# Performance work log

Hardware: AMD Instinct MI355X
Metric: run time of the kernel (lower is better)

## Reference

```python
import jax, jax.numpy as jnp
import numpy as np


def _piecewise_weights(gt):
    # stats over gt[0,0]; torch.std uses ddof=1
    g00 = gt[0, 0]
    gmin = jnp.min(g00)
    gmean = jnp.mean(g00)
    gmax = jnp.max(g00)
    sd = jnp.std(g00, ddof=1)
    m1 = gmean + sd
    m2 = gmean + 3.0 * sd
    w_low = (gt - gmin) / (m1 - gmin) * 0.2
    w_mid = (gt - m1) / (m2 - m1) * 0.5 + 0.2
    w_high = (gt - m2) / (gmax - m2) * 0.3 + 0.7
    return jnp.where(gt <= m1, w_low, jnp.where(gt <= m2, w_mid, w_high))


def setup_inputs() -> dict:
    key = jax.random.key(0)
    k1, k2 = jax.random.split(key)
    shape = (1, 1, 4096, 4096)
    inputs = jax.random.normal(k1, shape, dtype=jnp.float32)
    targets = jax.random.normal(k2, shape, dtype=jnp.float32)
    return {"inputs": inputs, "targets": targets}


def reference(inputs, targets):
    # gt is a detached clone of targets -> no grad through the weights
    gt = jax.lax.stop_gradient(targets)
    weights = _piecewise_weights(gt)
    loss = jnp.abs(targets - inputs)
    return jnp.mean(loss * weights)
```

## Files before the change

kernel.cpp:

```cpp
#include <hip/hip_runtime.h>
#include <math.h>

#define BS 256
#define NB 2048
#define NWAVES (BS / 64)
#define TBS 1024
#define TNW (TBS / 64)

__device__ inline double wred_sum(double v) {
#pragma unroll
    for (int o = 32; o > 0; o >>= 1) v += __shfl_down(v, o, 64);
    return v;
}
__device__ inline float wred_min(float v) {
#pragma unroll
    for (int o = 32; o > 0; o >>= 1) v = fminf(v, __shfl_down(v, o, 64));
    return v;
}
__device__ inline float wred_max(float v) {
#pragma unroll
    for (int o = 32; o > 0; o >>= 1) v = fmaxf(v, __shfl_down(v, o, 64));
    return v;
}

__global__ void __launch_bounds__(BS) k_stats(
        const float* __restrict__ t, int n,
        double* __restrict__ bsum, double* __restrict__ bss,
        float* __restrict__ bmn, float* __restrict__ bmx) {
    int tid = blockIdx.x * BS + threadIdx.x;
    const int stride = NB * BS;
    int n4 = n >> 2;
    const float4* t4 = (const float4*)t;

    double s = 0.0, ss = 0.0;
    float mn = 3.4e38f, mx = -3.4e38f;
    int i = tid;
    for (; i + stride < n4; i += 2 * stride) {
        float4 a = t4[i];
        float4 b = t4[i + stride];
        mn = fminf(mn, fminf(fminf(a.x, a.y), fminf(a.z, a.w)));
        mx = fmaxf(mx, fmaxf(fmaxf(a.x, a.y), fmaxf(a.z, a.w)));
        s += (double)a.x + (double)a.y + (double)a.z + (double)a.w;
        ss += (double)a.x * a.x + (double)a.y * a.y
            + (double)a.z * a.z + (double)a.w * a.w;
        mn = fminf(mn, fminf(fminf(b.x, b.y), fminf(b.z, b.w)));
        mx = fmaxf(mx, fmaxf(fmaxf(b.x, b.y), fmaxf(b.z, b.w)));
        s += (double)b.x + (double)b.y + (double)b.z + (double)b.w;
        ss += (double)b.x * b.x + (double)b.y * b.y
            + (double)b.z * b.z + (double)b.w * b.w;
    }
    for (; i < n4; i += stride) {
        float4 a = t4[i];
        mn = fminf(mn, fminf(fminf(a.x, a.y), fminf(a.z, a.w)));
        mx = fmaxf(mx, fmaxf(fmaxf(a.x, a.y), fmaxf(a.z, a.w)));
        s += (double)a.x + (double)a.y + (double)a.z + (double)a.w;
        ss += (double)a.x * a.x + (double)a.y * a.y
            + (double)a.z * a.z + (double)a.w * a.w;
    }
    if (tid == 0) {
        for (int j = (n4 << 2); j < n; j++) {
            float v = t[j];
            mn = fminf(mn, v); mx = fmaxf(mx, v);
            s += v; ss += (double)v * v;
        }
    }

    s = wred_sum(s); ss = wred_sum(ss); mn = wred_min(mn); mx = wred_max(mx);

    __shared__ double sh_s[NWAVES], sh_ss[NWAVES];
    __shared__ float sh_mn[NWAVES], sh_mx[NWAVES];
    int wid = threadIdx.x >> 6, lane = threadIdx.x & 63;
    if (lane == 0) { sh_s[wid] = s; sh_ss[wid] = ss; sh_mn[wid] = mn; sh_mx[wid] = mx; }
    __syncthreads();
    if (threadIdx.x == 0) {
        double S = sh_s[0], SS = sh_ss[0];
        float MN = sh_mn[0], MX = sh_mx[0];
        for (int k = 1; k < NWAVES; k++) {
            S += sh_s[k]; SS += sh_ss[k];
            MN = fminf(MN, sh_mn[k]); MX = fmaxf(MX, sh_mx[k]);
        }
        bsum[blockIdx.x] = S; bss[blockIdx.x] = SS;
        bmn[blockIdx.x] = MN; bmx[blockIdx.x] = MX;
    }
}

__device__ inline float welem(float g, float x, float gmin, float m1, float m2,
                              float sl, float sm, float shv) {
    float w = (g <= m1) ? (g - gmin) * sl
            : (g <= m2) ? (g - m1) * sm + 0.2f
                        : (g - m2) * shv + 0.7f;
    return fabsf(g - x) * w;
}

__global__ void __launch_bounds__(BS) k_loss(
        const float* __restrict__ x, const float* __restrict__ t, int n,
        const double* __restrict__ sbsum, const double* __restrict__ sbss,
        const float* __restrict__ sbmn, const float* __restrict__ sbmx,
        double* __restrict__ bsum) {
    __shared__ double sh_s[NWAVES], sh_ss[NWAVES];
    __shared__ float sh_mn[NWAVES], sh_mx[NWAVES];
    __shared__ float s_c[8];
    {
        double s = 0.0, ss = 0.0;
        float mn = 3.4e38f, mx = -3.4e38f;
        for (int i = threadIdx.x; i < NB; i += BS) {
            s += sbsum[i]; ss += sbss[i];
            mn = fminf(mn, sbmn[i]); mx = fmaxf(mx, sbmx[i]);
        }
        s = wred_sum(s); ss = wred_sum(ss); mn = wred_min(mn); mx = wred_max(mx);
        int wid = threadIdx.x >> 6, lane = threadIdx.x & 63;
        if (lane == 0) { sh_s[wid] = s; sh_ss[wid] = ss; sh_mn[wid] = mn; sh_mx[wid] = mx; }
        __syncthreads();
        if (threadIdx.x == 0) {
            double S = sh_s[0], SS = sh_ss[0];
            float MN = sh_mn[0], MX = sh_mx[0];
            for (int k = 1; k < NWAVES; k++) {
                S += sh_s[k]; SS += sh_ss[k];
                MN = fminf(MN, sh_mn[k]); MX = fmaxf(MX, sh_mx[k]);
            }
            double dn = (double)n;
            double mean = S / dn;
            double var = (SS - S * S / dn) / (dn - 1.0);
            double sd = sqrt(var);
            float m1 = (float)(mean + sd);
            float m2 = (float)(mean + 3.0 * sd);
            s_c[0] = MN;
            s_c[1] = m1;
            s_c[2] = m2;
            s_c[3] = 0.2f / (m1 - MN);
            s_c[4] = 0.5f / (m2 - m1);
            s_c[5] = 0.3f / (MX - m2);
        }
        __syncthreads();
    }
    float gmin = s_c[0], m1 = s_c[1], m2 = s_c[2];
    float sl = s_c[3], sm = s_c[4], shv = s_c[5];

    int tid = blockIdx.x * BS + threadIdx.x;
    const int stride = NB * BS;
    int n4 = n >> 2;
    const float4* x4 = (const float4*)x;
    const float4* t4 = (const float4*)t;

    double acc = 0.0;
    int i = tid;
    for (; i + stride < n4; i += 2 * stride) {
        float4 tv = t4[i], xv = x4[i];
        float4 tw = t4[i + stride], xw = x4[i + stride];
        float e0 = welem(tv.x, xv.x, gmin, m1, m2, sl, sm, shv);
        float e1 = welem(tv.y, xv.y, gmin, m1, m2, sl, sm, shv);
        float e2 = welem(tv.z, xv.z, gmin, m1, m2, sl, sm, shv);
        float e3 = welem(tv.w, xv.w, gmin, m1, m2, sl, sm, shv);
        acc += (double)e0 + (double)e1 + (double)e2 + (double)e3;
        float f0 = welem(tw.x, xw.x, gmin, m1, m2, sl, sm, shv);
        float f1 = welem(tw.y, xw.y, gmin, m1, m2, sl, sm, shv);
        float f2 = welem(tw.z, xw.z, gmin, m1, m2, sl, sm, shv);
        float f3 = welem(tw.w, xw.w, gmin, m1, m2, sl, sm, shv);
        acc += (double)f0 + (double)f1 + (double)f2 + (double)f3;
    }
    for (; i < n4; i += stride) {
        float4 tv = t4[i], xv = x4[i];
        float e0 = welem(tv.x, xv.x, gmin, m1, m2, sl, sm, shv);
        float e1 = welem(tv.y, xv.y, gmin, m1, m2, sl, sm, shv);
        float e2 = welem(tv.z, xv.z, gmin, m1, m2, sl, sm, shv);
        float e3 = welem(tv.w, xv.w, gmin, m1, m2, sl, sm, shv);
        acc += (double)e0 + (double)e1 + (double)e2 + (double)e3;
    }
    if (tid == 0) {
        for (int j = (n4 << 2); j < n; j++)
            acc += (double)welem(t[j], x[j], gmin, m1, m2, sl, sm, shv);
    }

    acc = wred_sum(acc);
    __shared__ double sh_acc[NWAVES];
    int wid = threadIdx.x >> 6, lane = threadIdx.x & 63;
    if (lane == 0) sh_acc[wid] = acc;
    __syncthreads();
    if (threadIdx.x == 0) {
        double S = sh_acc[0];
        for (int k = 1; k < NWAVES; k++) S += sh_acc[k];
        bsum[blockIdx.x] = S;
    }
}

__global__ void __launch_bounds__(TBS) k_final(
        const double* __restrict__ bsum, long long n, float* __restrict__ out) {
    double s = 0.0;
    for (int i = threadIdx.x; i < NB; i += TBS) s += bsum[i];
    s = wred_sum(s);
    __shared__ double sh_s[TNW];
    int wid = threadIdx.x >> 6, lane = threadIdx.x & 63;
    if (lane == 0) sh_s[wid] = s;
    __syncthreads();
    if (threadIdx.x == 0) {
        double S = sh_s[0];
        for (int i = 1; i < TNW; i++) S += sh_s[i];
        out[0] = (float)(S / (double)n);
    }
}

extern "C" void kernel_launch(void* const* d_in, const int* in_sizes, int n_in,
                              void* d_out, int out_size, void* d_ws, size_t ws_size,
                              hipStream_t stream) {
    const float* inp = (const float*)d_in[0];
    const float* tgt = (const float*)d_in[1];
    int n = in_sizes[0];

    char* ws = (char*)d_ws;
    double* sum1  = (double*)(ws);
    double* ss1   = (double*)(ws + 16384);
    float*  mn1   = (float*)(ws + 32768);
    float*  mx1   = (float*)(ws + 40960);
    double* sum2  = (double*)(ws + 49280);

    k_stats<<<NB, BS, 0, stream>>>(tgt, n, sum1, ss1, mn1, mx1);
    k_loss<<<NB, BS, 0, stream>>>(inp, tgt, n, sum1, ss1, mn1, mx1, sum2);
    k_final<<<1, TBS, 0, stream>>>(sum2, (long long)n, (float*)d_out);
}
```

Before: 46.64 us.

## Fuse final reduction into loss kernel via fixed-point slotted atomics

Removes the third k_final launch. Each loss block adds its partial sum as a fixed-point integer into one of 64 padded atomic slots and bumps a per-slot counter. The last block to arrive in each slot waits until all counters sum to the block count, then reduces the slots and writes the output. The grid is also halved to 1024 blocks with a 4x unrolled load loop, and the slots are zeroed by block 0 of the stats kernel. This trades a kernel launch for atomic traffic and a spin-wait, and the fixed-point scaling limits precision and range.

After: 46.95 us. No clear change (+0.7%).

```diff
diff --git a/kernel.cpp b/kernel.cpp
--- a/kernel.cpp
+++ b/kernel.cpp
@@ -2,10 +2,12 @@
 #include <math.h>
 
 #define BS 256
-#define NB 2048
+#define NBLK 1024
 #define NWAVES (BS / 64)
-#define TBS 1024
-#define TNW (TBS / 64)
+#define NSLOT 64
+#define PER_SLOT (NBLK / NSLOT)
+#define FXS 4294967296.0
+
 
 __device__ inline double wred_sum(double v) {
 #pragma unroll
@@ -21,41 +23,49 @@
 #pragma unroll
     for (int o = 32; o > 0; o >>= 1) v = fmaxf(v, __shfl_down(v, o, 64));
     return v;
+}
+
+__device__ inline void acc_stats(float4 v, double& s, double& ss, float& mn, float& mx) {
+    mn = fminf(mn, fminf(fminf(v.x, v.y), fminf(v.z, v.w)));
+    mx = fmaxf(mx, fmaxf(fmaxf(v.x, v.y), fmaxf(v.z, v.w)));
+    s += (double)v.x + (double)v.y + (double)v.z + (double)v.w;
+    ss += (double)v.x * v.x + (double)v.y * v.y
+        + (double)v.z * v.z + (double)v.w * v.w;
 }
 
 __global__ void __launch_bounds__(BS) k_stats(
         const float* __restrict__ t, int n,
         double* __restrict__ bsum, double* __restrict__ bss,
-        float* __restrict__ bmn, float* __restrict__ bmx) {
+        float* __restrict__ bmn, float* __restrict__ bmx,
+        char* __restrict__ slots) {
+    if (blockIdx.x == 0) {
+        if (threadIdx.x < NSLOT)
+            *(long long*)(slots + (size_t)threadIdx.x * 128) = 0ll;
+        else if (threadIdx.x < 2 * NSLOT)
+            *(unsigned*)(slots + 8192 + (size_t)(threadIdx.x - NSLOT) * 128) = 0u;
+    }
+
     int tid = blockIdx.x * BS + threadIdx.x;
-    const int stride = NB * BS;
+    const int stride = NBLK * BS;
     int n4 = n >> 2;
     const float4* t4 = (const float4*)t;
 
     double s = 0.0, ss = 0.0;
     float mn = 3.4e38f, mx = -3.4e38f;
     int i = tid;
-    for (; i + stride < n4; i += 2 * stride) {
+    for (; i + 3 * stride < n4; i += 4 * stride) {
         float4 a = t4[i];
         float4 b = t4[i + stride];
-        mn = fminf(mn, fminf(fminf(a.x, a.y), fminf(a.z, a.w)));
-        mx = fmaxf(mx, fmaxf(fmaxf(a.x, a.y), fmaxf(a.z, a.w)));
-        s += (double)a.x + (double)a.y + (double)a.z + (double)a.w;
-        ss += (double)a.x * a.x + (double)a.y * a.y
-            + (double)a.z * a.z + (double)a.w * a.w;
-        mn = fminf(mn, fminf(fminf(b.x, b.y), fminf(b.z, b.w)));
-        mx = fmaxf(mx, fmaxf(fmaxf(b.x, b.y), fmaxf(b.z, b.w)));
-        s += (double)b.x + (double)b.y + (double)b.z + (double)b.w;
-        ss += (double)b.x * b.x + (double)b.y * b.y
-            + (double)b.z * b.z + (double)b.w * b.w;
+        float4 c = t4[i + 2 * stride];
+        float4 d = t4[i + 3 * stride];
+        acc_stats(a, s, ss, mn, mx);
+        acc_stats(b, s, ss, mn, mx);
+        acc_stats(c, s, ss, mn, mx);
+        acc_stats(d, s, ss, mn, mx);
     }
     for (; i < n4; i += stride) {
         float4 a = t4[i];
-        mn = fminf(mn, fminf(fminf(a.x, a.y), fminf(a.z, a.w)));
-        mx = fmaxf(mx, fmaxf(fmaxf(a.x, a.y), fmaxf(a.z, a.w)));
-        s += (double)a.x + (double)a.y + (double)a.z + (double)a.w;
-        ss += (double)a.x * a.x + (double)a.y * a.y
-            + (double)a.z * a.z + (double)a.w * a.w;
+        acc_stats(a, s, ss, mn, mx);
     }
     if (tid == 0) {
         for (int j = (n4 << 2); j < n; j++) {
@@ -96,14 +106,15 @@
         const float* __restrict__ x, const float* __restrict__ t, int n,
         const double* __restrict__ sbsum, const double* __restrict__ sbss,
         const float* __restrict__ sbmn, const float* __restrict__ sbmx,
-        double* __restrict__ bsum) {
+        char* __restrict__ slots, float* __restrict__ out) {
     __shared__ double sh_s[NWAVES], sh_ss[NWAVES];
     __shared__ float sh_mn[NWAVES], sh_mx[NWAVES];
     __shared__ float s_c[8];
     {
         double s = 0.0, ss = 0.0;
         float mn = 3.4e38f, mx = -3.4e38f;
-        for (int i = threadIdx.x; i < NB; i += BS) {
+#pragma unroll 4
+        for (int i = threadIdx.x; i < NBLK; i += BS) {
             s += sbsum[i]; ss += sbss[i];
             mn = fminf(mn, sbmn[i]); mx = fmaxf(mx, sbmx[i]);
         }
@@ -137,34 +148,47 @@
     float sl = s_c[3], sm = s_c[4], shv = s_c[5];
 
     int tid = blockIdx.x * BS + threadIdx.x;
-    const int stride = NB * BS;
+    const int stride = NBLK * BS;
     int n4 = n >> 2;
     const float4* x4 = (const float4*)x;
     const float4* t4 = (const float4*)t;
 
     double acc = 0.0;
     int i = tid;
-    for (; i + stride < n4; i += 2 * stride) {
-        float4 tv = t4[i], xv = x4[i];
-        float4 tw = t4[i + stride], xw = x4[i + stride];
-        float e0 = welem(tv.x, xv.x, gmin, m1, m2, sl, sm, shv);
-        float e1 = welem(tv.y, xv.y, gmin, m1, m2, sl, sm, shv);
-        float e2 = welem(tv.z, xv.z, gmin, m1, m2, sl, sm, shv);
-        float e3 = welem(tv.w, xv.w, gmin, m1, m2, sl, sm, shv);
+    for (; i + 3 * stride < n4; i += 4 * stride) {
+        float4 t0 = t4[i];
+        float4 t1 = t4[i + stride];
+        float4 t2 = t4[i + 2 * stride];
+        float4 t3 = t4[i + 3 * stride];
+        float4 x0 = x4[i];
+        float4 x1 = x4[i + stride];
+        float4 x2 = x4[i + 2 * stride];
+        float4 x3 = x4[i + 3 * stride];
+        float e0 = welem(t0.x, x0.x, gmin, m1, m2, sl, sm, shv)
+                 + welem(t0.y, x0.y, gmin, m1, m2, sl, sm, shv)
+                 + welem(t0.z, x0.z, gmin, m1, m2, sl, sm, shv)
+                 + welem(t0.w, x0.w, gmin, m1, m2, sl, sm, shv);
+        float e1 = welem(t1.x, x1.x, gmin, m1, m2, sl, sm, shv)
+                 + welem(t1.y, x1.y, gmin, m1, m2, sl, sm, shv)
+                 + welem(t1.z, x1.z, gmin, m1, m2, sl, sm, shv)
+                 + welem(t1.w, x1.w, gmin, m1, m2, sl, sm, shv);
+        float e2 = welem(t2.x, x2.x, gmin, m1, m2, sl, sm, shv)
+                 + welem(t2.y, x2.y, gmin, m1, m2, sl, sm, shv)
+                 + welem(t2.z, x2.z, gmin, m1, m2, sl, sm, shv)
+                 + welem(t2.w, x2.w, gmin, m1, m2, sl, sm, shv);
+        float e3 = welem(t3.x, x3.x, gmin, m1, m2, sl, sm, shv)
+                 + welem(t3.y, x3.y, gmin, m1, m2, sl, sm, shv)
+                 + welem(t3.z, x3.z, gmin, m1, m2, sl, sm, shv)
+                 + welem(t3.w, x3.w, gmin, m1, m2, sl, sm, shv);
         acc += (double)e0 + (double)e1 + (double)e2 + (double)e3;
-        float f0 = welem(tw.x, xw.x, gmin, m1, m2, sl, sm, shv);
-        float f1 = welem(tw.y, xw.y, gmin, m1, m2, sl, sm, shv);
-        float f2 = welem(tw.z, xw.z, gmin, m1, m2, sl, sm, shv);
-        float f3 = welem(tw.w, xw.w, gmin, m1, m2, sl, sm, shv);
-        acc += (double)f0 + (double)f1 + (double)f2 + (double)f3;
     }
     for (; i < n4; i += stride) {
         float4 tv = t4[i], xv = x4[i];
-        float e0 = welem(tv.x, xv.x, gmin, m1, m2, sl, sm, shv);
-        float e1 = welem(tv.y, xv.y, gmin, m1, m2, sl, sm, shv);
-        float e2 = welem(tv.z, xv.z, gmin, m1, m2, sl, sm, shv);
-        float e3 = welem(tv.w, xv.w, gmin, m1, m2, sl, sm, shv);
-        acc += (double)e0 + (double)e1 + (double)e2 + (double)e3;
+        float e0 = welem(tv.x, xv.x, gmin, m1, m2, sl, sm, shv)
+                 + welem(tv.y, xv.y, gmin, m1, m2, sl, sm, shv)
+                 + welem(tv.z, xv.z, gmin, m1, m2, sl, sm, shv)
+                 + welem(tv.w, xv.w, gmin, m1, m2, sl, sm, shv);
+        acc += (double)e0;
     }
     if (tid == 0) {
         for (int j = (n4 << 2); j < n; j++)
@@ -173,29 +197,44 @@
 
     acc = wred_sum(acc);
     __shared__ double sh_acc[NWAVES];
+    __shared__ int s_fin;
     int wid = threadIdx.x >> 6, lane = threadIdx.x & 63;
     if (lane == 0) sh_acc[wid] = acc;
     __syncthreads();
     if (threadIdx.x == 0) {
         double S = sh_acc[0];
         for (int k = 1; k < NWAVES; k++) S += sh_acc[k];
-        bsum[blockIdx.x] = S;
-    }
-}
-
-__global__ void __launch_bounds__(TBS) k_final(
-        const double* __restrict__ bsum, long long n, float* __restrict__ out) {
-    double s = 0.0;
-    for (int i = threadIdx.x; i < NB; i += TBS) s += bsum[i];
-    s = wred_sum(s);
-    __shared__ double sh_s[TNW];
-    int wid = threadIdx.x >> 6, lane = threadIdx.x & 63;
-    if (lane == 0) sh_s[wid] = s;
+        int slot = blockIdx.x & (NSLOT - 1);
+        long long* lslot = (long long*)(slots + (size_t)slot * 128);
+        unsigned*  cslot = (unsigned*)(slots + 8192 + (size_t)slot * 128);
+        __hip_atomic_fetch_add(lslot, (long long)llrint(S * FXS),
+                               __ATOMIC_RELAXED, __HIP_MEMORY_SCOPE_AGENT);
+        asm volatile("s_waitcnt vmcnt(0)" ::: "memory");
+        unsigned prev = __hip_atomic_fetch_add(cslot, 1u,
+                               __ATOMIC_RELAXED, __HIP_MEMORY_SCOPE_AGENT);
+        s_fin = (prev == PER_SLOT - 1) ? 1 : 0;
+    }
     __syncthreads();
-    if (threadIdx.x == 0) {
-        double S = sh_s[0];
-        for (int i = 1; i < TNW; i++) S += sh_s[i];
-        out[0] = (float)(S / (double)n);
+    if (!s_fin) return;
+
+    if (threadIdx.x < 64) {
+        unsigned total;
+        do {
+            unsigned c = __hip_atomic_load(
+                (unsigned*)(slots + 8192 + (size_t)threadIdx.x * 128),
+                __ATOMIC_RELAXED, __HIP_MEMORY_SCOPE_AGENT);
+#pragma unroll
+            for (int o = 32; o > 0; o >>= 1) c += __shfl_down(c, o, 64);
+            total = __shfl(c, 0, 64);
+            if (total != NBLK) __builtin_amdgcn_s_sleep(32);
+        } while (total != NBLK);
+        long long v = __hip_atomic_load(
+            (long long*)(slots + (size_t)threadIdx.x * 128),
+            __ATOMIC_RELAXED, __HIP_MEMORY_SCOPE_AGENT);
+#pragma unroll
+        for (int o = 32; o > 0; o >>= 1) v += __shfl_down(v, o, 64);
+        if (threadIdx.x == 0)
+            out[0] = (float)(((double)v / FXS) / (double)n);
     }
 }
 
@@ -207,13 +246,13 @@
     int n = in_sizes[0];
 
     char* ws = (char*)d_ws;
-    double* sum1  = (double*)(ws);
-    double* ss1   = (double*)(ws + 16384);
-    float*  mn1   = (float*)(ws + 32768);
-    float*  mx1   = (float*)(ws + 40960);
-    double* sum2  = (double*)(ws + 49280);
-
-    k_stats<<<NB, BS, 0, stream>>>(tgt, n, sum1, ss1, mn1, mx1);
-    k_loss<<<NB, BS, 0, stream>>>(inp, tgt, n, sum1, ss1, mn1, mx1, sum2);
-    k_final<<<1, TBS, 0, stream>>>(sum2, (long long)n, (float*)d_out);
-}
+    double* bsum = (double*)(ws);
+    double* bss  = (double*)(ws + 8192);
+    float*  bmn  = (float*)(ws + 16384);
+    float*  bmx  = (float*)(ws + 20480);
+    char*   slots = ws + 24576;
+
+    k_stats<<<NBLK, BS, 0, stream>>>(tgt, n, bsum, bss, bmn, bmx, slots);
+    k_loss<<<NBLK, BS, 0, stream>>>(inp, tgt, n, bsum, bss, bmn, bmx,
+                                    slots, (float*)d_out);
+}
```
